# Kernel optimization log

Hardware: AMD Instinct MI355X
Metric: run time of the kernel (lower is better)

## Reference

```python
import jax, jax.numpy as jnp
import numpy as np

N_NODES = 50000
N_EDGES = 800000
D = 128
E_DIM = 32
N_LAYERS = 4
BN_EPS = 1e-5


def setup_inputs() -> dict:
    key = jax.random.key(0)
    ks = jax.random.split(key, 9)
    return {
        "x": jax.random.normal(ks[0], (N_NODES, D), dtype=jnp.float32),
        "edge_attr": jax.random.normal(ks[1], (N_EDGES, E_DIM), dtype=jnp.float32),
        "edge_index": jax.random.randint(ks[2], (2, N_EDGES), 0, N_NODES, dtype=jnp.int64),
        "W_edge": jax.random.normal(ks[3], (N_LAYERS, E_DIM, D), dtype=jnp.float32) * 0.1,
        "b_edge": jnp.zeros((N_LAYERS, D), dtype=jnp.float32),
        "W1": jax.random.normal(ks[4], (N_LAYERS, D, D), dtype=jnp.float32) * 0.1,
        "b1": jnp.zeros((N_LAYERS, D), dtype=jnp.float32),
        "W2": jax.random.normal(ks[5], (N_LAYERS, D, D), dtype=jnp.float32) * 0.1,
        "b2": jnp.zeros((N_LAYERS, D), dtype=jnp.float32),
        "gamma": jnp.ones((N_LAYERS, D), dtype=jnp.float32),
        "beta": jnp.zeros((N_LAYERS, D), dtype=jnp.float32),
    }


def reference(x, edge_attr, edge_index, W_edge, b_edge, W1, b1, W2, b2, gamma, beta):
    src, dst = edge_index[0], edge_index[1]
    n = x.shape[0]
    for i in range(N_LAYERS):
        # GINEConv: message = ReLU(x_src + Lin(edge_attr)); scatter-add to dst
        e = edge_attr @ W_edge[i] + b_edge[i]            # [E, D]
        m = jax.nn.relu(x[src] + e)                      # [E, D]
        agg = jax.ops.segment_sum(m, dst, num_segments=n)  # [N, D]
        h = x + agg                                      # (1+eps)*x, eps=0
        # 2-layer MLP
        h = jax.nn.relu(h @ W1[i] + b1[i]) @ W2[i] + b2[i]
        # BatchNorm (training-mode batch stats, biased var) + ReLU; dropout off
        mean = h.mean(axis=0)
        var = h.var(axis=0)
        h = (h - mean) * jax.lax.rsqrt(var + BN_EPS) * gamma[i] + beta[i]
        x = jax.nn.relu(h)
    return x
```

## Files before the change

### kernel.cpp

```cpp
#include <hip/hip_runtime.h>

#define NN 50000
#define NE 800000
#define DD 128
#define ED 32
#define NL 4
#define BN_EPS 1e-5f
#define SCAN_B 1024
#define NB ((NN + SCAN_B - 1) / SCAN_B)
#define EB 128
#define MR 32

typedef __attribute__((ext_vector_type(8))) short bf16x8;
typedef __attribute__((ext_vector_type(4))) float f32x4;

__device__ __forceinline__ unsigned short f2bf(float f) {
    unsigned u = __float_as_uint(f);
    u += 0x7fffu + ((u >> 16) & 1u);
    return (unsigned short)(u >> 16);
}
__device__ __forceinline__ float bf2f(unsigned short h) {
    return __uint_as_float((unsigned)h << 16);
}

__global__ __launch_bounds__(256) void hist_kernel(
    const int* __restrict__ edst, int* __restrict__ deg)
{
    const int e = blockIdx.x * 256 + threadIdx.x;
    if (e < NE) atomicAdd(&deg[edst[e]], 1);
}

__global__ __launch_bounds__(256) void scan1_kernel(
    const int* __restrict__ deg, int* __restrict__ rowptr, int* __restrict__ bsum)
{
    __shared__ int sh[256];
    const int t = threadIdx.x, b = blockIdx.x;
    const int base = b * SCAN_B + t * 4;
    int v[4];
#pragma unroll
    for (int j = 0; j < 4; ++j) {
        const int idx = base + j;
        v[j] = (idx < NN) ? deg[idx] : 0;
    }
    sh[t] = v[0] + v[1] + v[2] + v[3];
    __syncthreads();
    for (int off = 1; off < 256; off <<= 1) {
        const int val = (t >= off) ? sh[t - off] : 0;
        __syncthreads();
        sh[t] += val;
        __syncthreads();
    }
    int p = (t == 0) ? 0 : sh[t - 1];
#pragma unroll
    for (int j = 0; j < 4; ++j) {
        const int idx = base + j;
        if (idx < NN) rowptr[idx] = p;
        p += v[j];
    }
    if (t == 255) bsum[b] = sh[255];
}

__global__ void scan2_kernel(int* __restrict__ bsum)
{
    if (threadIdx.x == 0) {
        int acc = 0;
        for (int i = 0; i < NB; ++i) { const int v = bsum[i]; bsum[i] = acc; acc += v; }
    }
}

__global__ __launch_bounds__(256) void scan3_kernel(
    int* __restrict__ rowptr, int* __restrict__ cursor, const int* __restrict__ bsum)
{
    const int idx = blockIdx.x * 256 + threadIdx.x;
    if (idx < NN) {
        const int v = rowptr[idx] + bsum[idx / SCAN_B];
        rowptr[idx] = v;
        cursor[idx] = v;
    }
    if (idx == 0) rowptr[NN] = NE;
}

__global__ __launch_bounds__(256) void scatter_idx_kernel(
    const int* __restrict__ edst, int* __restrict__ cursor, int* __restrict__ eid_perm)
{
    const int e = blockIdx.x * 256 + threadIdx.x;
    if (e < NE) {
        const int pos = atomicAdd(&cursor[edst[e]], 1);
        eid_perm[pos] = e;
    }
}

__global__ __launch_bounds__(256) void sdea_kernel(
    const int* __restrict__ eid_perm, const int* __restrict__ esrc,
    const int* __restrict__ edst, const float* __restrict__ ea,
    int2* __restrict__ sd_perm, unsigned short* __restrict__ ea_bf)
{
    const int tid = blockIdx.x * 256 + threadIdx.x;
    const int pos = tid >> 3, j = tid & 7;
    if (pos < NE) {
        const int e = eid_perm[pos];
        if (j == 0) sd_perm[pos] = make_int2(esrc[e], edst[e]);
        const float4 v = *(const float4*)&ea[(size_t)e * ED + j * 4];
        uint2 p;
        p.x = (unsigned)f2bf(v.x) | ((unsigned)f2bf(v.y) << 16);
        p.y = (unsigned)f2bf(v.z) | ((unsigned)f2bf(v.w) << 16);
        *(uint2*)&ea_bf[(size_t)pos * ED + j * 4] = p;
    }
    if (tid == 0) sd_perm[NE] = make_int2(0, -1);
}

__global__ __launch_bounds__(256) void x0conv_kernel(
    const float* __restrict__ x0, unsigned short* __restrict__ xbf)
{
    const size_t i = ((size_t)blockIdx.x * 256 + threadIdx.x) * 8;
    if (i >= (size_t)NN * DD) return;
    const float4 a = *(const float4*)&x0[i];
    const float4 b = *(const float4*)&x0[i + 4];
    uint4 o;
    o.x = (unsigned)f2bf(a.x) | ((unsigned)f2bf(a.y) << 16);
    o.y = (unsigned)f2bf(a.z) | ((unsigned)f2bf(a.w) << 16);
    o.z = (unsigned)f2bf(b.x) | ((unsigned)f2bf(b.y) << 16);
    o.w = (unsigned)f2bf(b.z) | ((unsigned)f2bf(b.w) << 16);
    *(uint4*)&xbf[i] = o;
}

__global__ __launch_bounds__(256) void wconv_kernel(
    const float* __restrict__ We, unsigned short* __restrict__ wtb)
{
    const int tid = blockIdx.x * 256 + threadIdx.x;
    if (tid < NL * DD * ED) {
        const int l = tid / (DD * ED);
        const int r = tid % (DD * ED);
        const int c = r / ED, k = r % ED;
        wtb[tid] = f2bf(We[(size_t)l * ED * DD + k * DD + c]);
    }
}

__global__ __launch_bounds__(256) void w12conv_kernel(
    const float* __restrict__ W1, const float* __restrict__ W2,
    unsigned short* __restrict__ w1t, unsigned short* __restrict__ w2t)
{
    const int tid = blockIdx.x * 256 + threadIdx.x;
    if (tid < NL * DD * DD) {
        const int l = tid / (DD * DD);
        const int r = tid % (DD * DD);
        const int n = r / DD, k = r % DD;
        const size_t s = (size_t)l * DD * DD + k * DD + n;
        w1t[tid] = f2bf(W1[s]);
        w2t[tid] = f2bf(W2[s]);
    }
}

__global__ __launch_bounds__(256, 5) void edge_mfma_kernel(
    const unsigned short* __restrict__ xbf,
    const unsigned short* __restrict__ eab,
    const int2* __restrict__ sd_perm,
    const unsigned short* __restrict__ wtb,
    const float* __restrict__ be,
    float* __restrict__ agg)
{
    __shared__ unsigned short msgl[EB * 128];
    const int t = threadIdx.x;
    const int wv = t >> 6, ln = t & 63;
    const int l15 = ln & 15, kb = ln >> 4;

    const int nwg = NE / EB;
    const int q = nwg >> 3, r = nwg & 7;
    const int xcd = blockIdx.x & 7, seq = blockIdx.x >> 3;
    const int wg = (xcd < r ? xcd * (q + 1) : r * (q + 1) + (xcd - r) * q) + seq;
    const int e0 = wg * EB;

    const int c0 = (2 * wv + 0) * 16 + l15;
    const int c1 = (2 * wv + 1) * 16 + l15;
    const bf16x8 bfr0 = *(const bf16x8*)&wtb[c0 * ED + kb * 8];
    const bf16x8 bfr1 = *(const bf16x8*)&wtb[c1 * ED + kb * 8];

#pragma unroll
    for (int eg = 0; eg < EB / 16; ++eg) {
        const int edge = eg * 16 + l15;
        const bf16x8 afr = *(const bf16x8*)&eab[(size_t)(e0 + edge) * ED + kb * 8];
        f32x4 z = {0.f, 0.f, 0.f, 0.f};
        const f32x4 d0 = __builtin_amdgcn_mfma_f32_16x16x32_bf16(afr, bfr0, z, 0, 0, 0);
        const f32x4 d1 = __builtin_amdgcn_mfma_f32_16x16x32_bf16(afr, bfr1, z, 0, 0, 0);
#pragma unroll
        for (int j = 0; j < 4; ++j) {
            const int mrow = eg * 16 + kb * 4 + j;
            const int sw = ((mrow >> 2) & 3) << 3;
            const int i0 = (((c0 >> 1) ^ sw) << 1) | (c0 & 1);
            const int i1 = (((c1 >> 1) ^ sw) << 1) | (c1 & 1);
            msgl[mrow * 128 + i0] = f2bf(d0[j]);
            msgl[mrow * 128 + i1] = f2bf(d1[j]);
        }
    }
    __syncthreads();

    const int lbase = wv * 32;
    const int2* sdp = &sd_perm[e0 + lbase];
    const int c2 = ln * 2;
    const float2 bv = *(const float2*)&be[c2];
    float2 acc = {0.f, 0.f};
    int seg_start = 0;
#pragma unroll 1
    for (int g = 0; g < 2; ++g) {
        const int gb = g * 16;
        int4 pr[8];
#pragma unroll
        for (int q2 = 0; q2 < 8; ++q2)
            pr[q2] = *(const int4*)&sdp[gb + 2 * q2];
        int srcs[16], dsts[17];
#pragma unroll
        for (int q2 = 0; q2 < 8; ++q2) {
            srcs[2 * q2] = pr[q2].x; srcs[2 * q2 + 1] = pr[q2].z;
            dsts[2 * q2] = pr[q2].y; dsts[2 * q2 + 1] = pr[q2].w;
        }
        dsts[16] = sdp[gb + 16].y;
        float2 xv[16];
#pragma unroll
        for (int q2 = 0; q2 < 16; ++q2) {
            const unsigned xu = *(const unsigned*)&xbf[(size_t)srcs[q2] * DD + c2];
            xv[q2].x = __uint_as_float(xu << 16);
            xv[q2].y = __uint_as_float(xu & 0xffff0000u);
        }
#pragma unroll
        for (int q2 = 0; q2 < 16; ++q2) {
            const int i = gb + q2;
            const int dw = ln ^ (((i >> 2) & 3) << 3);
            const unsigned mm = *(const unsigned*)&msgl[(lbase + i) * 128 + dw * 2];
            const float mlo = __uint_as_float(mm << 16);
            const float mhi = __uint_as_float(mm & 0xffff0000u);
            acc.x += fmaxf(xv[q2].x + mlo + bv.x, 0.f);
            acc.y += fmaxf(xv[q2].y + mhi + bv.y, 0.f);
            if (i == 31 || dsts[q2 + 1] != dsts[q2]) {
                float* ap = &agg[(size_t)dsts[q2] * DD + c2];
                if (seg_start > 0 && i < 31) {
                    *(float2*)ap = acc;
                } else {
                    unsafeAtomicAdd(ap + 0, acc.x);
                    unsafeAtomicAdd(ap + 1, acc.y);
                }
                acc.x = 0.f; acc.y = 0.f;
                seg_start = i + 1;
            }
        }
    }
}

__global__ __launch_bounds__(256, 5) void mlp_mfma_kernel(
    const unsigned short* __restrict__ xbf, const float* __restrict__ agg,
    float* __restrict__ h2out,
    const unsigned short* __restrict__ w1t,
    const unsigned short* __restrict__ w2t,
    const float* __restrict__ b1, const float* __restrict__ b2,
    float* __restrict__ bns)
{
    __shared__ unsigned short ah[MR * 128];
    __shared__ unsigned short al[MR * 128];
    __shared__ unsigned short bh[MR * 128];
    const int t = threadIdx.x;
    const int wv = t >> 6, ln = t & 63, l15 = ln & 15, kb = ln >> 4;
    const int r0 = blockIdx.x * MR;

#pragma unroll
    for (int p = 0; p < 2; ++p) {
        const int row = p * 16 + (t >> 4);
        const int gc = t & 15;
        const int grow = r0 + row;
        float v[8] = {0.f, 0.f, 0.f, 0.f, 0.f, 0.f, 0.f, 0.f};
        if (grow < NN) {
            const size_t g = (size_t)grow * DD + gc * 8;
            const uint4 xu = *(const uint4*)&xbf[g];
            const float4 ga = *(const float4*)&agg[g];
            const float4 gb4 = *(const float4*)&agg[g + 4];
            v[0] = __uint_as_float(xu.x << 16)          + ga.x;
            v[1] = __uint_as_float(xu.x & 0xffff0000u)  + ga.y;
            v[2] = __uint_as_float(xu.y << 16)          + ga.z;
            v[3] = __uint_as_float(xu.y & 0xffff0000u)  + ga.w;
            v[4] = __uint_as_float(xu.z << 16)          + gb4.x;
            v[5] = __uint_as_float(xu.z & 0xffff0000u)  + gb4.y;
            v[6] = __uint_as_float(xu.w << 16)          + gb4.z;
            v[7] = __uint_as_float(xu.w & 0xffff0000u)  + gb4.w;
        }
        unsigned hiw[4], low[4];
#pragma unroll
        for (int j = 0; j < 4; ++j) {
            const unsigned short h0 = f2bf(v[2 * j]);
            const unsigned short h1 = f2bf(v[2 * j + 1]);
            const unsigned short q0 = f2bf(v[2 * j] - bf2f(h0));
            const unsigned short q1 = f2bf(v[2 * j + 1] - bf2f(h1));
            hiw[j] = (unsigned)h0 | ((unsigned)h1 << 16);
            low[j] = (unsigned)q0 | ((unsigned)q1 << 16);
        }
        const int off = row * 128 + (gc ^ (row & 7)) * 8;
        *(uint4*)&ah[off] = *(uint4*)hiw;
        *(uint4*)&al[off] = *(uint4*)low;
    }

    bf16x8 w1f[2][4];
#pragma unroll
    for (int nt = 0; nt < 2; ++nt) {
        const int n = wv * 32 + nt * 16 + l15;
#pragma unroll
        for (int ks = 0; ks < 4; ++ks)
            w1f[nt][ks] = *(const bf16x8*)&w1t[n * DD + ks * 32 + kb * 8];
    }
    const int cA = wv * 32 + l15, cB = wv * 32 + 16 + l15;
    const float b1v[2] = {b1[cA], b1[cB]};
    const float b2v[2] = {b2[cA], b2[cB]};
    __syncthreads();

    f32x4 acc[2][2];
#pragma unroll
    for (int mt = 0; mt < 2; ++mt)
#pragma unroll
        for (int nt = 0; nt < 2; ++nt)
            acc[mt][nt] = (f32x4){0.f, 0.f, 0.f, 0.f};
#pragma unroll
    for (int ks = 0; ks < 4; ++ks) {
#pragma unroll
        for (int mt = 0; mt < 2; ++mt) {
            const int row = mt * 16 + l15;
            const int off = row * 128 + ((ks * 4 + kb) ^ (row & 7)) * 8;
            const bf16x8 afh = *(const bf16x8*)&ah[off];
            const bf16x8 afl = *(const bf16x8*)&al[off];
#pragma unroll
            for (int nt = 0; nt < 2; ++nt) {
                acc[mt][nt] = __builtin_amdgcn_mfma_f32_16x16x32_bf16(afh, w1f[nt][ks], acc[mt][nt], 0, 0, 0);
                acc[mt][nt] = __builtin_amdgcn_mfma_f32_16x16x32_bf16(afl, w1f[nt][ks], acc[mt][nt], 0, 0, 0);
            }
        }
    }

#pragma unroll
    for (int mt = 0; mt < 2; ++mt) {
#pragma unroll
        for (int nt = 0; nt < 2; ++nt) {
            const int col = wv * 32 + nt * 16 + l15;
#pragma unroll
            for (int j = 0; j < 4; ++j) {
                const int row = mt * 16 + kb * 4 + j;
                const float v = fmaxf(acc[mt][nt][j] + b1v[nt], 0.f);
                const int off = row * 128 + ((col >> 3) ^ (row & 7)) * 8 + (col & 7);
                bh[off] = f2bf(v);
            }
        }
    }

    bf16x8 w2f[2][4];
#pragma unroll
    for (int nt = 0; nt < 2; ++nt) {
        const int n = wv * 32 + nt * 16 + l15;
#pragma unroll
        for (int ks = 0; ks < 4; ++ks)
            w2f[nt][ks] = *(const bf16x8*)&w2t[n * DD + ks * 32 + kb * 8];
    }
    __syncthreads();

#pragma unroll
    for (int mt = 0; mt < 2; ++mt)
#pragma unroll
        for (int nt = 0; nt < 2; ++nt)
            acc[mt][nt] = (f32x4){0.f, 0.f, 0.f, 0.f};
#pragma unroll
    for (int ks = 0; ks < 4; ++ks) {
#pragma unroll
        for (int mt = 0; mt < 2; ++mt) {
            const int row = mt * 16 + l15;
            const int off = row * 128 + ((ks * 4 + kb) ^ (row & 7)) * 8;
            const bf16x8 afh = *(const bf16x8*)&bh[off];
#pragma unroll
            for (int nt = 0; nt < 2; ++nt)
                acc[mt][nt] = __builtin_amdgcn_mfma_f32_16x16x32_bf16(afh, w2f[nt][ks], acc[mt][nt], 0, 0, 0);
        }
    }

    float ps[2] = {0.f, 0.f}, pq[2] = {0.f, 0.f};
#pragma unroll
    for (int mt = 0; mt < 2; ++mt) {
#pragma unroll
        for (int nt = 0; nt < 2; ++nt) {
            const int col = wv * 32 + nt * 16 + l15;
#pragma unroll
            for (int j = 0; j < 4; ++j) {
                const int row = r0 + mt * 16 + kb * 4 + j;
                const float v = acc[mt][nt][j] + b2v[nt];
                if (row < NN) {
                    h2out[(size_t)row * DD + col] = v;
                    ps[nt] += v;
                    pq[nt] += v * v;
                }
            }
        }
    }
#pragma unroll
    for (int nt = 0; nt < 2; ++nt) {
        ps[nt] += __shfl_xor(ps[nt], 16);
        ps[nt] += __shfl_xor(ps[nt], 32);
        pq[nt] += __shfl_xor(pq[nt], 16);
        pq[nt] += __shfl_xor(pq[nt], 32);
    }
    if (kb == 0) {
#pragma unroll
        for (int nt = 0; nt < 2; ++nt) {
            const int col = wv * 32 + nt * 16 + l15;
            unsafeAtomicAdd(&bns[col], ps[nt]);
            unsafeAtomicAdd(&bns[DD + col], pq[nt]);
        }
    }
}

__global__ __launch_bounds__(256) void bn_apply_bf16(
    float* __restrict__ h2, const float* __restrict__ bns,
    const float* __restrict__ gamma, const float* __restrict__ beta,
    unsigned short* __restrict__ xout)
{
    const size_t i = ((size_t)blockIdx.x * 256 + threadIdx.x) * 4;
    if (i >= (size_t)NN * DD) return;
    const int c4 = (int)(i & 127);
    const float4 hv = *(const float4*)&h2[i];
    const float4 sv = *(const float4*)&bns[c4];
    const float4 qv = *(const float4*)&bns[DD + c4];
    const float4 gv = *(const float4*)&gamma[c4];
    const float4 bv = *(const float4*)&beta[c4];
    const float inv_n = 1.f / (float)NN;
    float o0, o1, o2, o3;
    { const float m = sv.x * inv_n; const float var = qv.x * inv_n - m * m;
      o0 = fmaxf((hv.x - m) * __frsqrt_rn(var + BN_EPS) * gv.x + bv.x, 0.f); }
    { const float m = sv.y * inv_n; const float var = qv.y * inv_n - m * m;
      o1 = fmaxf((hv.y - m) * __frsqrt_rn(var + BN_EPS) * gv.y + bv.y, 0.f); }
    { const float m = sv.z * inv_n; const float var = qv.z * inv_n - m * m;
      o2 = fmaxf((hv.z - m) * __frsqrt_rn(var + BN_EPS) * gv.z + bv.z, 0.f); }
    { const float m = sv.w * inv_n; const float var = qv.w * inv_n - m * m;
      o3 = fmaxf((hv.w - m) * __frsqrt_rn(var + BN_EPS) * gv.w + bv.w, 0.f); }
    uint2 o;
    o.x = (unsigned)f2bf(o0) | ((unsigned)f2bf(o1) << 16);
    o.y = (unsigned)f2bf(o2) | ((unsigned)f2bf(o3) << 16);
    *(uint2*)&xout[i] = o;
    *(float4*)&h2[i] = (float4){0.f, 0.f, 0.f, 0.f};
}

__global__ __launch_bounds__(256) void bn_apply_f32(
    const float* __restrict__ h2, const float* __restrict__ bns,
    const float* __restrict__ gamma, const float* __restrict__ beta,
    float* __restrict__ xout)
{
    const size_t i = ((size_t)blockIdx.x * 256 + threadIdx.x) * 4;
    if (i >= (size_t)NN * DD) return;
    const int c4 = (int)(i & 127);
    const float4 hv = *(const float4*)&h2[i];
    const float4 sv = *(const float4*)&bns[c4];
    const float4 qv = *(const float4*)&bns[DD + c4];
    const float4 gv = *(const float4*)&gamma[c4];
    const float4 bv = *(const float4*)&beta[c4];
    const float inv_n = 1.f / (float)NN;
    float4 ov;
    { const float m = sv.x * inv_n; const float var = qv.x * inv_n - m * m;
      ov.x = fmaxf((hv.x - m) * __frsqrt_rn(var + BN_EPS) * gv.x + bv.x, 0.f); }
    { const float m = sv.y * inv_n; const float var = qv.y * inv_n - m * m;
      ov.y = fmaxf((hv.y - m) * __frsqrt_rn(var + BN_EPS) * gv.y + bv.y, 0.f); }
    { const float m = sv.z * inv_n; const float var = qv.z * inv_n - m * m;
      ov.z = fmaxf((hv.z - m) * __frsqrt_rn(var + BN_EPS) * gv.z + bv.z, 0.f); }
    { const float m = sv.w * inv_n; const float var = qv.w * inv_n - m * m;
      ov.w = fmaxf((hv.w - m) * __frsqrt_rn(var + BN_EPS) * gv.w + bv.w, 0.f); }
    *(float4*)&xout[i] = ov;
}

extern "C" void kernel_launch(void* const* d_in, const int* in_sizes, int n_in,
                              void* d_out, int out_size, void* d_ws, size_t ws_size,
                              hipStream_t stream) {
    const float* x0    = (const float*)d_in[0];
    const float* ea    = (const float*)d_in[1];
    const int*   eidx  = (const int*)d_in[2];
    const float* We    = (const float*)d_in[3];
    const float* be    = (const float*)d_in[4];
    const float* W1    = (const float*)d_in[5];
    const float* b1    = (const float*)d_in[6];
    const float* W2    = (const float*)d_in[7];
    const float* b2    = (const float*)d_in[8];
    const float* gamma = (const float*)d_in[9];
    const float* beta  = (const float*)d_in[10];
    float* out = (float*)d_out;
    float* ws  = (float*)d_ws;

    float* agg = ws;
    float* bns = agg + (size_t)NN * DD;
    int* deg      = (int*)(bns + NL * 256);
    int* rowptr   = deg + 50000;
    int* cursor   = rowptr + 50004;
    int* bsum     = cursor + 50000;
    int2* sd_perm = (int2*)(bsum + 64);
    int* eid_perm = (int*)(sd_perm + NE + 2);
    unsigned short* ea_bf = (unsigned short*)(eid_perm + NE);
    unsigned short* wt_bf = ea_bf + (size_t)NE * ED;
    unsigned short* w1t   = wt_bf + (size_t)NL * DD * ED;
    unsigned short* w2t   = w1t + (size_t)NL * DD * DD;
    unsigned short* xbf   = w2t + (size_t)NL * DD * DD;

    const int* esrc = eidx;
    const int* edst = eidx + NE;

    hipMemsetAsync(deg, 0, NN * sizeof(int), stream);
    hipMemsetAsync(bns, 0, NL * 256 * sizeof(float), stream);
    hipMemsetAsync(agg, 0, (size_t)NN * DD * sizeof(float), stream);
    hist_kernel<<<(NE + 255) / 256, 256, 0, stream>>>(edst, deg);
    scan1_kernel<<<NB, 256, 0, stream>>>(deg, rowptr, bsum);
    scan2_kernel<<<1, 64, 0, stream>>>(bsum);
    scan3_kernel<<<(NN + 255) / 256, 256, 0, stream>>>(rowptr, cursor, bsum);
    scatter_idx_kernel<<<(NE + 255) / 256, 256, 0, stream>>>(edst, cursor, eid_perm);
    sdea_kernel<<<((size_t)NE * 8 + 255) / 256, 256, 0, stream>>>(
        eid_perm, esrc, edst, ea, sd_perm, ea_bf);
    x0conv_kernel<<<((NN * DD / 8) + 255) / 256, 256, 0, stream>>>(x0, xbf);
    wconv_kernel<<<(NL * DD * ED + 255) / 256, 256, 0, stream>>>(We, wt_bf);
    w12conv_kernel<<<(NL * DD * DD + 255) / 256, 256, 0, stream>>>(W1, W2, w1t, w2t);

    for (int l = 0; l < NL; ++l) {
        edge_mfma_kernel<<<NE / EB, 256, 0, stream>>>(
            xbf, ea_bf, sd_perm,
            wt_bf + (size_t)l * DD * ED, be + (size_t)l * DD, agg);
        mlp_mfma_kernel<<<(NN + MR - 1) / MR, 256, 0, stream>>>(
            xbf, agg, agg,
            w1t + (size_t)l * DD * DD, w2t + (size_t)l * DD * DD,
            b1 + (size_t)l * DD, b2 + (size_t)l * DD, bns + l * 256);
        if (l < NL - 1) {
            bn_apply_bf16<<<(NN * DD / 4 + 255) / 256, 256, 0, stream>>>(
                agg, bns + l * 256, gamma + (size_t)l * DD, beta + (size_t)l * DD, xbf);
        } else {
            bn_apply_f32<<<(NN * DD / 4 + 255) / 256, 256, 0, stream>>>(
                agg, bns + l * 256, gamma + (size_t)l * DD, beta + (size_t)l * DD, out);
        }
    }
}
```

Baseline: 664.1 us.

## Batch all edge source gathers up front and make MLP kernel grid-stride persistent

In the edge kernel, each wave now loads all 32 src/dst pairs and issues all 32 x-row gathers before the accumulate loop, instead of two sequential batches of 16. This exposes more memory-level parallelism to hide gather latency, at the cost of more registers, so the occupancy hint drops from 5 to 4. The MLP kernel becomes a grid-stride loop over a fixed grid of 1280 blocks, loading the W1 and W2 fragments once per block and reusing them across tiles. With 1563 tiles and 1280 blocks, some blocks process two tiles while others process one, which may leave the tail unbalanced.

```diff
diff --git a/kernel.cpp b/kernel.cpp
--- a/kernel.cpp
+++ b/kernel.cpp
@@ -10,6 +10,7 @@
 #define NB ((NN + SCAN_B - 1) / SCAN_B)
 #define EB 128
 #define MR 32
+#define MLP_GRID 1280
 
 typedef __attribute__((ext_vector_type(8))) short bf16x8;
 typedef __attribute__((ext_vector_type(4))) float f32x4;
@@ -151,7 +152,7 @@
     }
 }
 
-__global__ __launch_bounds__(256, 5) void edge_mfma_kernel(
+__global__ __launch_bounds__(256, 4) void edge_mfma_kernel(
     const unsigned short* __restrict__ xbf,
     const unsigned short* __restrict__ eab,
     const int2* __restrict__ sd_perm,
@@ -198,49 +199,45 @@
     const int2* sdp = &sd_perm[e0 + lbase];
     const int c2 = ln * 2;
     const float2 bv = *(const float2*)&be[c2];
+
+    int4 pr[16];
+#pragma unroll
+    for (int q2 = 0; q2 < 16; ++q2)
+        pr[q2] = *(const int4*)&sdp[2 * q2];
+    int dsts[33];
+#pragma unroll
+    for (int q2 = 0; q2 < 16; ++q2) {
+        dsts[2 * q2]     = pr[q2].y;
+        dsts[2 * q2 + 1] = pr[q2].w;
+    }
+    dsts[32] = sdp[32].y;
+    unsigned xu[32];
+#pragma unroll
+    for (int q2 = 0; q2 < 16; ++q2) {
+        xu[2 * q2]     = *(const unsigned*)&xbf[(size_t)pr[q2].x * DD + c2];
+        xu[2 * q2 + 1] = *(const unsigned*)&xbf[(size_t)pr[q2].z * DD + c2];
+    }
+
     float2 acc = {0.f, 0.f};
     int seg_start = 0;
-#pragma unroll 1
-    for (int g = 0; g < 2; ++g) {
-        const int gb = g * 16;
-        int4 pr[8];
-#pragma unroll
-        for (int q2 = 0; q2 < 8; ++q2)
-            pr[q2] = *(const int4*)&sdp[gb + 2 * q2];
-        int srcs[16], dsts[17];
-#pragma unroll
-        for (int q2 = 0; q2 < 8; ++q2) {
-            srcs[2 * q2] = pr[q2].x; srcs[2 * q2 + 1] = pr[q2].z;
-            dsts[2 * q2] = pr[q2].y; dsts[2 * q2 + 1] = pr[q2].w;
-        }
-        dsts[16] = sdp[gb + 16].y;
-        float2 xv[16];
-#pragma unroll
-        for (int q2 = 0; q2 < 16; ++q2) {
-            const unsigned xu = *(const unsigned*)&xbf[(size_t)srcs[q2] * DD + c2];
-            xv[q2].x = __uint_as_float(xu << 16);
-            xv[q2].y = __uint_as_float(xu & 0xffff0000u);
-        }
-#pragma unroll
-        for (int q2 = 0; q2 < 16; ++q2) {
-            const int i = gb + q2;
-            const int dw = ln ^ (((i >> 2) & 3) << 3);
-            const unsigned mm = *(const unsigned*)&msgl[(lbase + i) * 128 + dw * 2];
-            const float mlo = __uint_as_float(mm << 16);
-            const float mhi = __uint_as_float(mm & 0xffff0000u);
-            acc.x += fmaxf(xv[q2].x + mlo + bv.x, 0.f);
-            acc.y += fmaxf(xv[q2].y + mhi + bv.y, 0.f);
-            if (i == 31 || dsts[q2 + 1] != dsts[q2]) {
-                float* ap = &agg[(size_t)dsts[q2] * DD + c2];
-                if (seg_start > 0 && i < 31) {
-                    *(float2*)ap = acc;
-                } else {
-                    unsafeAtomicAdd(ap + 0, acc.x);
-                    unsafeAtomicAdd(ap + 1, acc.y);
-                }
-                acc.x = 0.f; acc.y = 0.f;
-                seg_start = i + 1;
-            }
+#pragma unroll
+    for (int i = 0; i < 32; ++i) {
+        const int dw = ln ^ (((i >> 2) & 3) << 3);
+        const unsigned mm = *(const unsigned*)&msgl[(lbase + i) * 128 + dw * 2];
+        const float mlo = __uint_as_float(mm << 16);
+        const float mhi = __uint_as_float(mm & 0xffff0000u);
+        acc.x += fmaxf(__uint_as_float(xu[i] << 16) + mlo + bv.x, 0.f);
+        acc.y += fmaxf(__uint_as_float(xu[i] & 0xffff0000u) + mhi + bv.y, 0.f);
+        if (i == 31 || dsts[i + 1] != dsts[i]) {
+            float* ap = &agg[(size_t)dsts[i] * DD + c2];
+            if (seg_start > 0 && i < 31) {
+                *(float2*)ap = acc;
+            } else {
+                unsafeAtomicAdd(ap + 0, acc.x);
+                unsafeAtomicAdd(ap + 1, acc.y);
+            }
+            acc.x = 0.f; acc.y = 0.f;
+            seg_start = i + 1;
         }
     }
 }
@@ -258,152 +255,149 @@
     __shared__ unsigned short bh[MR * 128];
     const int t = threadIdx.x;
     const int wv = t >> 6, ln = t & 63, l15 = ln & 15, kb = ln >> 4;
-    const int r0 = blockIdx.x * MR;
-
-#pragma unroll
-    for (int p = 0; p < 2; ++p) {
-        const int row = p * 16 + (t >> 4);
-        const int gc = t & 15;
-        const int grow = r0 + row;
-        float v[8] = {0.f, 0.f, 0.f, 0.f, 0.f, 0.f, 0.f, 0.f};
-        if (grow < NN) {
-            const size_t g = (size_t)grow * DD + gc * 8;
-            const uint4 xu = *(const uint4*)&xbf[g];
-            const float4 ga = *(const float4*)&agg[g];
-            const float4 gb4 = *(const float4*)&agg[g + 4];
-            v[0] = __uint_as_float(xu.x << 16)          + ga.x;
-            v[1] = __uint_as_float(xu.x & 0xffff0000u)  + ga.y;
-            v[2] = __uint_as_float(xu.y << 16)          + ga.z;
-            v[3] = __uint_as_float(xu.y & 0xffff0000u)  + ga.w;
-            v[4] = __uint_as_float(xu.z << 16)          + gb4.x;
-            v[5] = __uint_as_float(xu.z & 0xffff0000u)  + gb4.y;
-            v[6] = __uint_as_float(xu.w << 16)          + gb4.z;
-            v[7] = __uint_as_float(xu.w & 0xffff0000u)  + gb4.w;
-        }
-        unsigned hiw[4], low[4];
-#pragma unroll
-        for (int j = 0; j < 4; ++j) {
-            const unsigned short h0 = f2bf(v[2 * j]);
-            const unsigned short h1 = f2bf(v[2 * j + 1]);
-            const unsigned short q0 = f2bf(v[2 * j] - bf2f(h0));
-            const unsigned short q1 = f2bf(v[2 * j + 1] - bf2f(h1));
-            hiw[j] = (unsigned)h0 | ((unsigned)h1 << 16);
-            low[j] = (unsigned)q0 | ((unsigned)q1 << 16);
-        }
-        const int off = row * 128 + (gc ^ (row & 7)) * 8;
-        *(uint4*)&ah[off] = *(uint4*)hiw;
-        *(uint4*)&al[off] = *(uint4*)low;
-    }
-
-    bf16x8 w1f[2][4];
+
+    bf16x8 w1f[2][4], w2f[2][4];
 #pragma unroll
     for (int nt = 0; nt < 2; ++nt) {
         const int n = wv * 32 + nt * 16 + l15;
 #pragma unroll
-        for (int ks = 0; ks < 4; ++ks)
+        for (int ks = 0; ks < 4; ++ks) {
             w1f[nt][ks] = *(const bf16x8*)&w1t[n * DD + ks * 32 + kb * 8];
+            w2f[nt][ks] = *(const bf16x8*)&w2t[n * DD + ks * 32 + kb * 8];
+        }
     }
     const int cA = wv * 32 + l15, cB = wv * 32 + 16 + l15;
     const float b1v[2] = {b1[cA], b1[cB]};
     const float b2v[2] = {b2[cA], b2[cB]};
-    __syncthreads();
-
-    f32x4 acc[2][2];
-#pragma unroll
-    for (int mt = 0; mt < 2; ++mt)
-#pragma unroll
-        for (int nt = 0; nt < 2; ++nt)
-            acc[mt][nt] = (f32x4){0.f, 0.f, 0.f, 0.f};
-#pragma unroll
-    for (int ks = 0; ks < 4; ++ks) {
+
+    const int NT = (NN + MR - 1) / MR;
+    for (int tile = blockIdx.x; tile < NT; tile += gridDim.x) {
+        const int r0 = tile * MR;
+
+#pragma unroll
+        for (int p = 0; p < 2; ++p) {
+            const int row = p * 16 + (t >> 4);
+            const int gc = t & 15;
+            const int grow = r0 + row;
+            float v[8] = {0.f, 0.f, 0.f, 0.f, 0.f, 0.f, 0.f, 0.f};
+            if (grow < NN) {
+                const size_t g = (size_t)grow * DD + gc * 8;
+                const uint4 xu = *(const uint4*)&xbf[g];
+                const float4 ga = *(const float4*)&agg[g];
+                const float4 gb4 = *(const float4*)&agg[g + 4];
+                v[0] = __uint_as_float(xu.x << 16)          + ga.x;
+                v[1] = __uint_as_float(xu.x & 0xffff0000u)  + ga.y;
+                v[2] = __uint_as_float(xu.y << 16)          + ga.z;
+                v[3] = __uint_as_float(xu.y & 0xffff0000u)  + ga.w;
+                v[4] = __uint_as_float(xu.z << 16)          + gb4.x;
+                v[5] = __uint_as_float(xu.z & 0xffff0000u)  + gb4.y;
+                v[6] = __uint_as_float(xu.w << 16)          + gb4.z;
+                v[7] = __uint_as_float(xu.w & 0xffff0000u)  + gb4.w;
+            }
+            unsigned hiw[4], low[4];
+#pragma unroll
+            for (int j = 0; j < 4; ++j) {
+                const unsigned short h0 = f2bf(v[2 * j]);
+                const unsigned short h1 = f2bf(v[2 * j + 1]);
+                const unsigned short q0 = f2bf(v[2 * j] - bf2f(h0));
+                const unsigned short q1 = f2bf(v[2 * j + 1] - bf2f(h1));
+                hiw[j] = (unsigned)h0 | ((unsigned)h1 << 16);
+                low[j] = (unsigned)q0 | ((unsigned)q1 << 16);
+            }
+            const int off = row * 128 + (gc ^ (row & 7)) * 8;
+            *(uint4*)&ah[off] = *(uint4*)hiw;
+            *(uint4*)&al[off] = *(uint4*)low;
+        }
+        __syncthreads();
+
+        f32x4 acc[2][2];
+#pragma unroll
+        for (int mt = 0; mt < 2; ++mt)
+#pragma unroll
+            for (int nt = 0; nt < 2; ++nt)
+                acc[mt][nt] = (f32x4){0.f, 0.f, 0.f, 0.f};
+#pragma unroll
+        for (int ks = 0; ks < 4; ++ks) {
+#pragma unroll
+            for (int mt = 0; mt < 2; ++mt) {
+                const int row = mt * 16 + l15;
+                const int off = row * 128 + ((ks * 4 + kb) ^ (row & 7)) * 8;
+                const bf16x8 afh = *(const bf16x8*)&ah[off];
+                const bf16x8 afl = *(const bf16x8*)&al[off];
+#pragma unroll
+                for (int nt = 0; nt < 2; ++nt) {
+                    acc[mt][nt] = __builtin_amdgcn_mfma_f32_16x16x32_bf16(afh, w1f[nt][ks], acc[mt][nt], 0, 0, 0);
+                    acc[mt][nt] = __builtin_amdgcn_mfma_f32_16x16x32_bf16(afl, w1f[nt][ks], acc[mt][nt], 0, 0, 0);
+                }
+            }
+        }
+
 #pragma unroll
         for (int mt = 0; mt < 2; ++mt) {
-            const int row = mt * 16 + l15;
-            const int off = row * 128 + ((ks * 4 + kb) ^ (row & 7)) * 8;
-            const bf16x8 afh = *(const bf16x8*)&ah[off];
-            const bf16x8 afl = *(const bf16x8*)&al[off];
 #pragma unroll
             for (int nt = 0; nt < 2; ++nt) {
-                acc[mt][nt] = __builtin_amdgcn_mfma_f32_16x16x32_bf16(afh, w1f[nt][ks], acc[mt][nt], 0, 0, 0);
-                acc[mt][nt] = __builtin_amdgcn_mfma_f32_16x16x32_bf16(afl, w1f[nt][ks], acc[mt][nt], 0, 0, 0);
-            }
-        }
-    }
-
-#pragma unroll
-    for (int mt = 0; mt < 2; ++mt) {
+                const int col = wv * 32 + nt * 16 + l15;
+#pragma unroll
+                for (int j = 0; j < 4; ++j) {
+                    const int row = mt * 16 + kb * 4 + j;
+                    const float v = fmaxf(acc[mt][nt][j] + b1v[nt], 0.f);
+                    const int off = row * 128 + ((col >> 3) ^ (row & 7)) * 8 + (col & 7);
+                    bh[off] = f2bf(v);
+                }
+            }
+        }
+        __syncthreads();
+
+#pragma unroll
+        for (int mt = 0; mt < 2; ++mt)
+#pragma unroll
+            for (int nt = 0; nt < 2; ++nt)
+                acc[mt][nt] = (f32x4){0.f, 0.f, 0.f, 0.f};
+#pragma unroll
+        for (int ks = 0; ks < 4; ++ks) {
+#pragma unroll
+            for (int mt = 0; mt < 2; ++mt) {
+                const int row = mt * 16 + l15;
+                const int off = row * 128 + ((ks * 4 + kb) ^ (row & 7)) * 8;
+                const bf16x8 afh = *(const bf16x8*)&bh[off];
+#pragma unroll
+                for (int nt = 0; nt < 2; ++nt)
+                    acc[mt][nt] = __builtin_amdgcn_mfma_f32_16x16x32_bf16(afh, w2f[nt][ks], acc[mt][nt], 0, 0, 0);
+            }
+        }
+
+        float ps[2] = {0.f, 0.f}, pq[2] = {0.f, 0.f};
+#pragma unroll
+        for (int mt = 0; mt < 2; ++mt) {
+#pragma unroll
+            for (int nt = 0; nt < 2; ++nt) {
+                const int col = wv * 32 + nt * 16 + l15;
+#pragma unroll
+                for (int j = 0; j < 4; ++j) {
+                    const int row = r0 + mt * 16 + kb * 4 + j;
+                    const float v = acc[mt][nt][j] + b2v[nt];
+                    if (row < NN) {
+                        h2out[(size_t)row * DD + col] = v;
+                        ps[nt] += v;
+                        pq[nt] += v * v;
+                    }
+                }
+            }
+        }
 #pragma unroll
         for (int nt = 0; nt < 2; ++nt) {
-            const int col = wv * 32 + nt * 16 + l15;
-#pragma unroll
-            for (int j = 0; j < 4; ++j) {
-                const int row = mt * 16 + kb * 4 + j;
-                const float v = fmaxf(acc[mt][nt][j] + b1v[nt], 0.f);
-                const int off = row * 128 + ((col >> 3) ^ (row & 7)) * 8 + (col & 7);
-                bh[off] = f2bf(v);
-            }
-        }
-    }
-
-    bf16x8 w2f[2][4];
-#pragma unroll
-    for (int nt = 0; nt < 2; ++nt) {
-        const int n = wv * 32 + nt * 16 + l15;
-#pragma unroll
-        for (int ks = 0; ks < 4; ++ks)
-            w2f[nt][ks] = *(const bf16x8*)&w2t[n * DD + ks * 32 + kb * 8];
-    }
-    __syncthreads();
-
-#pragma unroll
-    for (int mt = 0; mt < 2; ++mt)
-#pragma unroll
-        for (int nt = 0; nt < 2; ++nt)
-            acc[mt][nt] = (f32x4){0.f, 0.f, 0.f, 0.f};
-#pragma unroll
-    for (int ks = 0; ks < 4; ++ks) {
-#pragma unroll
-        for (int mt = 0; mt < 2; ++mt) {
-            const int row = mt * 16 + l15;
-            const int off = row * 128 + ((ks * 4 + kb) ^ (row & 7)) * 8;
-            const bf16x8 afh = *(const bf16x8*)&bh[off];
-#pragma unroll
-            for (int nt = 0; nt < 2; ++nt)
-                acc[mt][nt] = __builtin_amdgcn_mfma_f32_16x16x32_bf16(afh, w2f[nt][ks], acc[mt][nt], 0, 0, 0);
-        }
-    }
-
-    float ps[2] = {0.f, 0.f}, pq[2] = {0.f, 0.f};
-#pragma unroll
-    for (int mt = 0; mt < 2; ++mt) {
-#pragma unroll
-        for (int nt = 0; nt < 2; ++nt) {
-            const int col = wv * 32 + nt * 16 + l15;
-#pragma unroll
-            for (int j = 0; j < 4; ++j) {
-                const int row = r0 + mt * 16 + kb * 4 + j;
-                const float v = acc[mt][nt][j] + b2v[nt];
-                if (row < NN) {
-                    h2out[(size_t)row * DD + col] = v;
-                    ps[nt] += v;
-                    pq[nt] += v * v;
-                }
-            }
-        }
-    }
-#pragma unroll
-    for (int nt = 0; nt < 2; ++nt) {
-        ps[nt] += __shfl_xor(ps[nt], 16);
-        ps[nt] += __shfl_xor(ps[nt], 32);
-        pq[nt] += __shfl_xor(pq[nt], 16);
-        pq[nt] += __shfl_xor(pq[nt], 32);
-    }
-    if (kb == 0) {
-#pragma unroll
-        for (int nt = 0; nt < 2; ++nt) {
-            const int col = wv * 32 + nt * 16 + l15;
-            unsafeAtomicAdd(&bns[col], ps[nt]);
-            unsafeAtomicAdd(&bns[DD + col], pq[nt]);
+            ps[nt] += __shfl_xor(ps[nt], 16);
+            ps[nt] += __shfl_xor(ps[nt], 32);
+            pq[nt] += __shfl_xor(pq[nt], 16);
+            pq[nt] += __shfl_xor(pq[nt], 32);
+        }
+        if (kb == 0) {
+#pragma unroll
+            for (int nt = 0; nt < 2; ++nt) {
+                const int col = wv * 32 + nt * 16 + l15;
+                unsafeAtomicAdd(&bns[col], ps[nt]);
+                unsafeAtomicAdd(&bns[DD + col], pq[nt]);
+            }
         }
     }
 }
@@ -516,7 +510,7 @@
         edge_mfma_kernel<<<NE / EB, 256, 0, stream>>>(
             xbf, ea_bf, sd_perm,
             wt_bf + (size_t)l * DD * ED, be + (size_t)l * DD, agg);
-        mlp_mfma_kernel<<<(NN + MR - 1) / MR, 256, 0, stream>>>(
+        mlp_mfma_kernel<<<MLP_GRID, 256, 0, stream>>>(
             xbf, agg, agg,
             w1t + (size_t)l * DD * DD, w2t + (size_t)l * DD * DD,
             b1 + (size_t)l * DD, b2 + (size_t)l * DD, bns + l * 256);
```

After: 833.4 us. +25.5%, slower.
